# Optimization experiments

Hardware: AMD Instinct MI355X
Metric: run time of the kernel (lower is better)

The kernel has to match this reference:

```python
import jax, jax.numpy as jnp
import numpy as np

N_QUBITS = 4  # kernel 2x2 -> 4 pixels -> 4 qubits -> 4 PauliZ outputs
KH, KW = 2, 2
STRIDE = 2
OUT_CHANNELS = 4


def _cnot(state, c, t):
    # state: [P, 2,2,2,2]; qubit q lives on axis q+1
    ca, ta = c + 1, t + 1
    s0 = jax.lax.index_in_dim(state, 0, ca, keepdims=True)
    s1 = jnp.flip(jax.lax.index_in_dim(state, 1, ca, keepdims=True), axis=ta)
    return jnp.concatenate([s0, s1], axis=ca)


def _ry(state, theta_q, q):
    c, s = jnp.cos(theta_q / 2), jnp.sin(theta_q / 2)
    M = jnp.stack([jnp.stack([c, -s]), jnp.stack([s, c])])  # [2,2] real RY
    out = jnp.tensordot(M, state, axes=([1], [q + 1]))
    return jnp.moveaxis(out, 0, q + 1)


def _qnode(angles, theta):
    # angles: [P, 4] patch pixels used as RY embedding angles
    c, s = jnp.cos(angles / 2), jnp.sin(angles / 2)
    # product state |psi> = RY(a0)|0> x RY(a1)|0> x RY(a2)|0> x RY(a3)|0>
    state = jnp.einsum('pa,pb,pc,pd->pabcd',
                       jnp.stack([c[:, 0], s[:, 0]], -1),
                       jnp.stack([c[:, 1], s[:, 1]], -1),
                       jnp.stack([c[:, 2], s[:, 2]], -1),
                       jnp.stack([c[:, 3], s[:, 3]], -1))
    for q in range(N_QUBITS):            # entangling CNOT ring
        state = _cnot(state, q, (q + 1) % N_QUBITS)
    for q in range(N_QUBITS):            # trainable RY layer
        state = _ry(state, theta[q], q)
    p = state * state                    # real amplitudes -> probabilities
    outs = []
    for q in range(N_QUBITS):            # <Z_q> expectation values
        axes = tuple(a for a in range(1, N_QUBITS + 1) if a != q + 1)
        m = jnp.sum(p, axis=axes)        # [P, 2]
        outs.append(m[:, 0] - m[:, 1])
    return jnp.stack(outs, axis=-1)      # [P, 4]


def _quanv(xc, theta, out_per):
    # xc: [B, 1, H, W]; stride == kernel so unfold == blocked reshape
    B, _, H, W = xc.shape
    Ho, Wo = (H - KH) // STRIDE + 1, (W - KW) // STRIDE + 1
    # unfold ordering: patch pixels row-major (di*KW+dj), patches row-major over (Ho,Wo)
    patches = xc.reshape(B, Ho, KH, Wo, KW).transpose(0, 1, 3, 2, 4).reshape(B, Ho * Wo, KH * KW)
    # torch.stack over unbound patch dim puts L (patches) outermost: [L, B, 4]
    patches = patches.transpose(1, 0, 2).reshape(-1, KH * KW)  # [L*B, 4]
    vals = _qnode(patches, theta)                              # [L*B, 4]
    # faithful to the original raw .view of the contiguous [L, B, 4] buffer
    return vals.reshape(B, out_per, Ho, Wo)


def reference(x, theta):
    B, C, H, W = x.shape
    out_per = OUT_CHANNELS // C
    outs = [_quanv(x[:, c:c + 1], theta, out_per) for c in range(C)]
    return jnp.concatenate(outs, axis=1)


def setup_inputs() -> dict:
    key = jax.random.key(0)
    k1, k2 = jax.random.split(key)
    x = jax.random.normal(k1, (32, 1, 512, 512), dtype=jnp.float32)
    theta = jax.random.normal(k2, (4,), dtype=jnp.float32)
    return {"x": x, "theta": theta}
```

## Files before the change

kernel.cpp:

```cpp
#include <hip/hip_runtime.h>

#define BATCH 32
#define HH 512
#define WW 512
#define HO 256
#define WO 256
#define LTOT (HO * WO)

__global__ __launch_bounds__(256) void quanv_kernel(const float* __restrict__ x,
                                                    const float* __restrict__ theta,
                                                    float* __restrict__ out) {
    __shared__ float4 lds[1024];

    const int tid    = threadIdx.x;
    const int l0     = blockIdx.x * 32;
    const int irow   = l0 >> 8;
    const int j0     = l0 & 255;
    const int l_sub  = tid & 31;
    const int b_base = tid >> 5;

    float ct[4], st[4];
#pragma unroll
    for (int q = 0; q < 4; ++q) {
        float h = theta[q] * 0.5f;
        __sincosf(h, &st[q], &ct[q]);
    }

    const int j = j0 + l_sub;
    const int roff0 = (2 * irow) * WW + 2 * j;
    const int roff1 = roff0 + WW;

#pragma unroll
    for (int pp = 0; pp < 4; ++pp) {
        const int b = b_base + pp * 8;
        const float* xb = x + (size_t)b * (HH * WW);
        const float2 r0 = *(const float2*)(xb + roff0);
        const float2 r1 = *(const float2*)(xb + roff1);

        float a[4] = {r0.x, r0.y, r1.x, r1.y};
        float pc[4], ps[4];
#pragma unroll
        for (int k = 0; k < 4; ++k) {
            __sincosf(a[k] * 0.5f, &ps[k], &pc[k]);
        }

        float amp[16];
#pragma unroll
        for (int s = 0; s < 16; ++s) {
            float v = ((s & 8) ? ps[0] : pc[0]);
            v *= ((s & 4) ? ps[1] : pc[1]);
            v *= ((s & 2) ? ps[2] : pc[2]);
            v *= ((s & 1) ? ps[3] : pc[3]);
            amp[s] = v;
        }

#pragma unroll
        for (int g = 0; g < 4; ++g) {
            const int cb = 8 >> g;
            const int tb = 8 >> ((g + 1) & 3);
#pragma unroll
            for (int s = 0; s < 16; ++s) {
                if ((s & cb) && !(s & tb)) {
                    float tmp = amp[s];
                    amp[s] = amp[s ^ tb];
                    amp[s ^ tb] = tmp;
                }
            }
        }

#pragma unroll
        for (int q = 0; q < 4; ++q) {
            const int qb = 8 >> q;
            const float c = ct[q], sv = st[q];
#pragma unroll
            for (int s = 0; s < 16; ++s) {
                if (!(s & qb)) {
                    float v0 = amp[s], v1 = amp[s | qb];
                    amp[s]      = c * v0 - sv * v1;
                    amp[s | qb] = sv * v0 + c * v1;
                }
            }
        }

        float z0 = 0.f, z1 = 0.f, z2 = 0.f, z3 = 0.f;
#pragma unroll
        for (int s = 0; s < 16; ++s) {
            float p = amp[s] * amp[s];
            z0 += (s & 8) ? -p : p;
            z1 += (s & 4) ? -p : p;
            z2 += (s & 2) ? -p : p;
            z3 += (s & 1) ? -p : p;
        }

        lds[l_sub * 32 + (b ^ (l_sub & 7))] = make_float4(z0, z1, z2, z3);
    }

    __syncthreads();

    float4* out4 = (float4*)out + (size_t)l0 * 32;
#pragma unroll
    for (int k = 0; k < 4; ++k) {
        const int idx = k * 256 + tid;
        const int ls = idx >> 5, bb = idx & 31;
        out4[idx] = lds[ls * 32 + (bb ^ (ls & 7))];
    }
}

extern "C" void kernel_launch(void* const* d_in, const int* in_sizes, int n_in,
                              void* d_out, int out_size, void* d_ws, size_t ws_size,
                              hipStream_t stream) {
    const float* x     = (const float*)d_in[0];
    const float* theta = (const float*)d_in[1];
    float* out         = (float*)d_out;

    const int blocks = LTOT / 32;
    quanv_kernel<<<blocks, 256, 0, stream>>>(x, theta, out);
}
```

Baseline: 91.39 us.

## Process two patches per thread with float4 loads and hardware sin/cos

Each thread now handles two adjacent patches per batch, loading 16-byte float4 rows instead of 8-byte float2, and each block covers 64 patches with a doubled LDS staging buffer and a wider XOR swizzle. Trig calls switch from __sincosf to the raw AMDGCN sin/cos builtins, which take the argument pre-scaled by 1/(2π) (folded here with the half-angle as 1/(4π)). The aim is wider global loads, fewer blocks, and cheaper transcendental evaluation. The cost is more registers per thread, more LDS per block, and possible occupancy loss.

```diff
diff --git a/kernel.cpp b/kernel.cpp
--- a/kernel.cpp
+++ b/kernel.cpp
@@ -7,102 +7,112 @@
 #define WO 256
 #define LTOT (HO * WO)
 
+#define INV_4PI 0.07957747154594767f
+
 __global__ __launch_bounds__(256) void quanv_kernel(const float* __restrict__ x,
                                                     const float* __restrict__ theta,
                                                     float* __restrict__ out) {
-    __shared__ float4 lds[1024];
+    __shared__ float4 lds[2048];
 
-    const int tid    = threadIdx.x;
-    const int l0     = blockIdx.x * 32;
-    const int irow   = l0 >> 8;
-    const int j0     = l0 & 255;
-    const int l_sub  = tid & 31;
-    const int b_base = tid >> 5;
+    const int tid   = threadIdx.x;
+    const int l0    = blockIdx.x * 64;
+    const int irow  = l0 >> 8;
+    const int j0    = l0 & 255;
+    const int lpair = tid & 31;
+    const int b0    = tid >> 5;
 
     float ct[4], st[4];
 #pragma unroll
     for (int q = 0; q < 4; ++q) {
-        float h = theta[q] * 0.5f;
-        __sincosf(h, &st[q], &ct[q]);
+        const float r = theta[q] * INV_4PI;
+        st[q] = __builtin_amdgcn_sinf(r);
+        ct[q] = __builtin_amdgcn_cosf(r);
     }
 
-    const int j = j0 + l_sub;
-    const int roff0 = (2 * irow) * WW + 2 * j;
-    const int roff1 = roff0 + WW;
+    const int col  = 2 * (j0 + 2 * lpair);
+    const int off0 = (2 * irow) * WW + col;
+    const int off1 = off0 + WW;
 
 #pragma unroll
     for (int pp = 0; pp < 4; ++pp) {
-        const int b = b_base + pp * 8;
+        const int b = b0 + pp * 8;
         const float* xb = x + (size_t)b * (HH * WW);
-        const float2 r0 = *(const float2*)(xb + roff0);
-        const float2 r1 = *(const float2*)(xb + roff1);
-
-        float a[4] = {r0.x, r0.y, r1.x, r1.y};
-        float pc[4], ps[4];
-#pragma unroll
-        for (int k = 0; k < 4; ++k) {
-            __sincosf(a[k] * 0.5f, &ps[k], &pc[k]);
-        }
-
-        float amp[16];
-#pragma unroll
-        for (int s = 0; s < 16; ++s) {
-            float v = ((s & 8) ? ps[0] : pc[0]);
-            v *= ((s & 4) ? ps[1] : pc[1]);
-            v *= ((s & 2) ? ps[2] : pc[2]);
-            v *= ((s & 1) ? ps[3] : pc[3]);
-            amp[s] = v;
-        }
+        const float4 r0 = *(const float4*)(xb + off0);
+        const float4 r1 = *(const float4*)(xb + off1);
 
 #pragma unroll
-        for (int g = 0; g < 4; ++g) {
-            const int cb = 8 >> g;
-            const int tb = 8 >> ((g + 1) & 3);
+        for (int c = 0; c < 2; ++c) {
+            const float aa[4] = {c ? r0.z : r0.x, c ? r0.w : r0.y,
+                                 c ? r1.z : r1.x, c ? r1.w : r1.y};
+            float pc[4], ps[4];
+#pragma unroll
+            for (int k = 0; k < 4; ++k) {
+                const float r = aa[k] * INV_4PI;
+                ps[k] = __builtin_amdgcn_sinf(r);
+                pc[k] = __builtin_amdgcn_cosf(r);
+            }
+
+            float amp[16];
 #pragma unroll
             for (int s = 0; s < 16; ++s) {
-                if ((s & cb) && !(s & tb)) {
-                    float tmp = amp[s];
-                    amp[s] = amp[s ^ tb];
-                    amp[s ^ tb] = tmp;
+                float v = ((s & 8) ? ps[0] : pc[0]);
+                v *= ((s & 4) ? ps[1] : pc[1]);
+                v *= ((s & 2) ? ps[2] : pc[2]);
+                v *= ((s & 1) ? ps[3] : pc[3]);
+                amp[s] = v;
+            }
+
+#pragma unroll
+            for (int g = 0; g < 4; ++g) {
+                const int cb = 8 >> g;
+                const int tb = 8 >> ((g + 1) & 3);
+#pragma unroll
+                for (int s = 0; s < 16; ++s) {
+                    if ((s & cb) && !(s & tb)) {
+                        float tmp = amp[s];
+                        amp[s] = amp[s ^ tb];
+                        amp[s ^ tb] = tmp;
+                    }
                 }
             }
-        }
 
 #pragma unroll
-        for (int q = 0; q < 4; ++q) {
-            const int qb = 8 >> q;
-            const float c = ct[q], sv = st[q];
+            for (int q = 0; q < 4; ++q) {
+                const int qb = 8 >> q;
+                const float cc = ct[q], sv = st[q];
+#pragma unroll
+                for (int s = 0; s < 16; ++s) {
+                    if (!(s & qb)) {
+                        float v0 = amp[s], v1 = amp[s | qb];
+                        amp[s]      = cc * v0 - sv * v1;
+                        amp[s | qb] = sv * v0 + cc * v1;
+                    }
+                }
+            }
+
+            float z0 = 0.f, z1 = 0.f, z2 = 0.f, z3 = 0.f;
 #pragma unroll
             for (int s = 0; s < 16; ++s) {
-                if (!(s & qb)) {
-                    float v0 = amp[s], v1 = amp[s | qb];
-                    amp[s]      = c * v0 - sv * v1;
-                    amp[s | qb] = sv * v0 + c * v1;
-                }
+                float p = amp[s] * amp[s];
+                z0 += (s & 8) ? -p : p;
+                z1 += (s & 4) ? -p : p;
+                z2 += (s & 2) ? -p : p;
+                z3 += (s & 1) ? -p : p;
             }
+
+            const int lsub = 2 * lpair + c;
+            lds[lsub * 32 + (b ^ (lsub & 31))] = make_float4(z0, z1, z2, z3);
         }
-
-        float z0 = 0.f, z1 = 0.f, z2 = 0.f, z3 = 0.f;
-#pragma unroll
-        for (int s = 0; s < 16; ++s) {
-            float p = amp[s] * amp[s];
-            z0 += (s & 8) ? -p : p;
-            z1 += (s & 4) ? -p : p;
-            z2 += (s & 2) ? -p : p;
-            z3 += (s & 1) ? -p : p;
-        }
-
-        lds[l_sub * 32 + (b ^ (l_sub & 7))] = make_float4(z0, z1, z2, z3);
     }
 
     __syncthreads();
 
     float4* out4 = (float4*)out + (size_t)l0 * 32;
 #pragma unroll
-    for (int k = 0; k < 4; ++k) {
+    for (int k = 0; k < 8; ++k) {
         const int idx = k * 256 + tid;
         const int ls = idx >> 5, bb = idx & 31;
-        out4[idx] = lds[ls * 32 + (bb ^ (ls & 7))];
+        out4[idx] = lds[ls * 32 + (bb ^ (ls & 31))];
     }
 }
 
@@ -113,6 +123,6 @@
     const float* theta = (const float*)d_in[1];
     float* out         = (float*)d_out;
 
-    const int blocks = LTOT / 32;
+    const int blocks = LTOT / 64;
     quanv_kernel<<<blocks, 256, 0, stream>>>(x, theta, out);
 }
```

After: 91.58 us. About the same (+0.2%).
